# Kernel tuning notes

Hardware: AMD Instinct MI355X
Metric: run time of the kernel (lower is better)

Reference implementation:

```python
import jax, jax.numpy as jnp
import numpy as np

B, N, DIM = 1, 100_000, 512
HEADS, DIM_HEAD, M = 8, 64, 64


def setup_inputs() -> dict:
    key = jax.random.key(0)
    ks = jax.random.split(key, 9)
    s = 0.04  # ~ kaiming-ish scale for dim=512
    return {
        "x": jax.random.normal(ks[0], (B, N, DIM), dtype=jnp.float32),
        "temperature": jnp.full((1, HEADS, 1, 1), 0.5, dtype=jnp.float32),
        "w_slice": jax.random.normal(ks[1], (HEADS * M, DIM), dtype=jnp.float32) * s,
        "b_slice": jnp.zeros((HEADS * M,), dtype=jnp.float32),
        "w1": jax.random.normal(ks[2], (DIM_HEAD, DIM), dtype=jnp.float32) * s,
        "b1": jnp.zeros((DIM_HEAD,), dtype=jnp.float32),
        "wq": jax.random.normal(ks[3], (DIM_HEAD, DIM_HEAD), dtype=jnp.float32) * 0.125,
        "wk": jax.random.normal(ks[4], (DIM_HEAD, DIM_HEAD), dtype=jnp.float32) * 0.125,
        "wv": jax.random.normal(ks[5], (DIM_HEAD, DIM_HEAD), dtype=jnp.float32) * 0.125,
        "w3": jax.random.normal(ks[6], (DIM_HEAD, DIM_HEAD), dtype=jnp.float32) * 0.125,
        "b3": jnp.zeros((DIM_HEAD,), dtype=jnp.float32),
    }


def reference(x, temperature, w_slice, b_slice, w1, b1, wq, wk, wv, w3, b3):
    b, n, c = x.shape
    # slice logits: (B,N,H*M) -> (B,H,N,M)
    logits = jnp.einsum("bnc,ec->bne", x, w_slice) + b_slice
    logits = logits.reshape(b, n, HEADS, M).transpose(0, 2, 1, 3)
    temp = jnp.clip(temperature, 0.1, 5.0)
    w = jax.nn.softmax(logits / temp, axis=-1)          # (B,H,N,M)
    d = w.sum(axis=2)                                    # (B,H,M)
    # N -> M aggregation (w^T @ x per head)
    s_raw = jnp.einsum("bhnm,bnc->bhmc", w, x)          # (B,H,M,C)
    s = jnp.einsum("bhmc,dc->bhmd", s_raw / (d[..., None] + 1e-5), w1) + b1  # (B,H,M,dh)
    q = jnp.einsum("bhmd,ed->bhme", s, wq)
    k = jnp.einsum("bhmd,ed->bhme", s, wk)
    v = jnp.einsum("bhmd,ed->bhme", s, wv)
    scale = 1.0 / jnp.sqrt(jnp.asarray(DIM_HEAD, dtype=s.dtype))
    attn = jax.nn.softmax(jnp.einsum("bhme,bhle->bhml", q, k) * scale, axis=-1)
    s_att = jnp.einsum("bhml,bhle->bhme", attn, v)      # (B,H,M,dh)
    s_out = jnp.einsum("bhme,de->bhmd", s_att, w3) + b3
    # deslice: w @ s_out -> (B,H,N,dh) -> (B,N,H*dh)
    x_out = jnp.einsum("bhnm,bhmd->bhnd", w, s_out)
    return x_out.transpose(0, 2, 1, 3).reshape(b, n, HEADS * DIM_HEAD)
```

## Files before the change

kernel.cpp:

```cpp
#include <hip/hip_runtime.h>

typedef _Float16 f16;
typedef _Float16 f16x8 __attribute__((ext_vector_type(8)));
typedef _Float16 f16x4 __attribute__((ext_vector_type(4)));
typedef float    f32x4 __attribute__((ext_vector_type(4)));

#define N_TOK   100000
#define NPAD    100032
#define NT1     1563
#define NT4     1563
#define CDIM    512
#define KSTEPS  (NPAD/32)
#define K2SPL   128

#define O_WT     ((size_t)0)
#define SZ_WT    ((size_t)512*NPAD*2)
#define O_YT     (O_WT + SZ_WT)
#define SZ_YT    ((size_t)64*NPAD*2)
#define O_WFR    (O_YT + SZ_YT)
#define SZ_WFR   ((size_t)16*4*9*64*8*2)
#define O_SPP    (O_WFR + SZ_WFR)
#define SZ_SPP   ((size_t)K2SPL*32768*4)
#define O_DPP    (O_SPP + SZ_SPP)
#define SZ_DPP   ((size_t)K2SPL*512*4)
#define O_SPRE   (O_DPP + SZ_DPP)
#define SZ_SPRE  ((size_t)32768*4)
#define O_DSTD   (O_SPRE + SZ_SPRE)
#define SZ_DSTD  ((size_t)512*4)
#define O_SOUT   (O_DSTD + SZ_DSTD)

__global__ void k0_pack(const float* __restrict__ wsf, const float* __restrict__ w1f,
                        f16* __restrict__ wfr) {
    int c = blockIdx.x * 256 + threadIdx.x;
    int lane = c & 63, g = c >> 6;
    int u  = g % 9,  r = g / 9;
    int we = r & 3,  kg = r >> 2;
    int col = lane & 15, quad = lane >> 4;
    int k = kg * 32 + quad * 8;
    const float* src;
    if (u < 8) src = wsf + (size_t)(we*128 + u*16 + col) * CDIM + k;
    else       src = w1f + (size_t)(we*16  + col) * CDIM + k;
    float4 a = *(const float4*)(src);
    float4 b = *(const float4*)(src + 4);
    f16x8 h;
    h[0]=(f16)a.x; h[1]=(f16)a.y; h[2]=(f16)a.z; h[3]=(f16)a.w;
    h[4]=(f16)b.x; h[5]=(f16)b.y; h[6]=(f16)b.z; h[7]=(f16)b.w;
    *(f16x8*)(wfr + (size_t)c * 8) = h;
}

#define XROW 40
__launch_bounds__(256, 2)
__global__ void k1_slice(const float* __restrict__ x, const float* __restrict__ temperature,
                         const f16* __restrict__ wfr, const float* __restrict__ bsl,
                         f16* __restrict__ wT, f16* __restrict__ yT) {
    __shared__ f16 lX[2][64 * XROW];

    const int tid  = threadIdx.x;
    const int wave = tid >> 6;
    const int lane = tid & 63;
    const int quad = lane >> 4;
    const int col  = lane & 15;
    const int n0   = blockIdx.x * 64;

    const int srow = tid >> 2, sch = tid & 3;
    int snr = n0 + srow; if (snr > N_TOK - 1) snr = N_TOK - 1;
    const float* sbase = x + (size_t)snr * CDIM + sch * 8;

    {
        float4 a = *(const float4*)(sbase);
        float4 b = *(const float4*)(sbase + 4);
        f16x8 h;
        h[0]=(f16)a.x; h[1]=(f16)a.y; h[2]=(f16)a.z; h[3]=(f16)a.w;
        h[4]=(f16)b.x; h[5]=(f16)b.y; h[6]=(f16)b.z; h[7]=(f16)b.w;
        *(f16x8*)(&lX[0][srow * XROW + sch * 8]) = h;
    }

    f32x4 acc[4][9];
    #pragma unroll
    for (int nf = 0; nf < 4; ++nf)
        #pragma unroll
        for (int u = 0; u < 9; ++u) acc[nf][u] = f32x4{0.f,0.f,0.f,0.f};

    __syncthreads();

    #pragma unroll 2
    for (int kg = 0; kg < 16; ++kg) {
        const f16* wb = wfr + ((size_t)(kg*4 + wave) * 9) * 512 + (size_t)lane * 8;
        f16x8 bf[9];
        #pragma unroll
        for (int u = 0; u < 9; ++u) bf[u] = *(const f16x8*)(wb + u * 512);

        float4 xa, xb;
        if (kg < 15) {
            xa = *(const float4*)(sbase + (kg + 1) * 32);
            xb = *(const float4*)(sbase + (kg + 1) * 32 + 4);
        }

        const f16* xbuf = lX[kg & 1];
        f16x8 af[4];
        #pragma unroll
        for (int nf = 0; nf < 4; ++nf)
            af[nf] = *(const f16x8*)(xbuf + (nf*16 + col) * XROW + quad * 8);

        #pragma unroll
        for (int nf = 0; nf < 4; ++nf)
            #pragma unroll
            for (int u = 0; u < 9; ++u)
                acc[nf][u] = __builtin_amdgcn_mfma_f32_16x16x32_f16(af[nf], bf[u], acc[nf][u], 0, 0, 0);

        if (kg < 15) {
            f16x8 h;
            h[0]=(f16)xa.x; h[1]=(f16)xa.y; h[2]=(f16)xa.z; h[3]=(f16)xa.w;
            h[4]=(f16)xb.x; h[5]=(f16)xb.y; h[6]=(f16)xb.z; h[7]=(f16)xb.w;
            *(f16x8*)(&lX[(kg + 1) & 1][srow * XROW + sch * 8]) = h;
        }
        __syncthreads();
    }

    #pragma unroll
    for (int u = 0; u < 8; ++u) {
        float b = bsl[wave*128 + u*16 + col];
        #pragma unroll
        for (int nf = 0; nf < 4; ++nf)
            #pragma unroll
            for (int r = 0; r < 4; ++r) acc[nf][u][r] += b;
    }
    float invt[2];
    #pragma unroll
    for (int hh = 0; hh < 2; ++hh) {
        float tv = temperature[wave*2 + hh];
        tv = fminf(fmaxf(tv, 0.1f), 5.0f);
        invt[hh] = 1.0f / tv;
    }

    #pragma unroll
    for (int nf = 0; nf < 4; ++nf) {
        const int nb = n0 + nf*16 + quad*4;
        #pragma unroll
        for (int hh = 0; hh < 2; ++hh) {
            float mx[4];
            #pragma unroll
            for (int r = 0; r < 4; ++r) {
                float m01 = fmaxf(acc[nf][hh*4+0][r], acc[nf][hh*4+1][r]);
                float m23 = fmaxf(acc[nf][hh*4+2][r], acc[nf][hh*4+3][r]);
                mx[r] = fmaxf(m01, m23);
            }
            #pragma unroll
            for (int d = 1; d < 16; d <<= 1)
                #pragma unroll
                for (int r = 0; r < 4; ++r) mx[r] = fmaxf(mx[r], __shfl_xor(mx[r], d));
            float sm[4] = {0.f, 0.f, 0.f, 0.f};
            #pragma unroll
            for (int uu = 0; uu < 4; ++uu)
                #pragma unroll
                for (int r = 0; r < 4; ++r) {
                    float ev = __expf((acc[nf][hh*4+uu][r] - mx[r]) * invt[hh]);
                    acc[nf][hh*4+uu][r] = ev;
                    sm[r] += ev;
                }
            #pragma unroll
            for (int d = 1; d < 16; d <<= 1)
                #pragma unroll
                for (int r = 0; r < 4; ++r) sm[r] += __shfl_xor(sm[r], d);
            #pragma unroll
            for (int r = 0; r < 4; ++r) sm[r] = 1.0f / sm[r];
            #pragma unroll
            for (int uu = 0; uu < 4; ++uu) {
                f16x4 pk;
                #pragma unroll
                for (int r = 0; r < 4; ++r) {
                    int n = nb + r;
                    float wv = (n < N_TOK) ? acc[nf][hh*4+uu][r] * sm[r] : 0.0f;
                    pk[r] = (f16)wv;
                }
                int e = wave*128 + (hh*4 + uu)*16 + col;
                *(f16x4*)(wT + (size_t)e * NPAD + nb) = pk;
            }
        }
        {
            f16x4 pk;
            #pragma unroll
            for (int r = 0; r < 4; ++r) {
                int n = nb + r;
                pk[r] = (n < N_TOK) ? (f16)acc[nf][8][r] : (f16)0.f;
            }
            *(f16x4*)(yT + (size_t)(wave*16 + col) * NPAD + nb) = pk;
        }
    }
}

__launch_bounds__(256, 3)
__global__ void k2_spre(const f16* __restrict__ wT, const f16* __restrict__ yT,
                        float* __restrict__ spp, float* __restrict__ dpp) {
    const int tid = threadIdx.x, wave = tid >> 6, lane = tid & 63;
    const int quad = lane >> 4, col = lane & 15;
    const int slot = blockIdx.x >> 1, ehalf = blockIdx.x & 1;
    const int ebase = ehalf * 256 + wave * 64;

    f32x4 acc[4][4];
    float dac[4];
    #pragma unroll
    for (int u = 0; u < 4; ++u) {
        dac[u] = 0.f;
        #pragma unroll
        for (int v = 0; v < 4; ++v) acc[u][v] = f32x4{0.f,0.f,0.f,0.f};
    }
    for (int ks = slot; ks < KSTEPS; ks += K2SPL) {
        int nb = ks*32 + quad*8;
        f16x8 bf[4];
        #pragma unroll
        for (int v = 0; v < 4; ++v)
            bf[v] = *(const f16x8*)(yT + (size_t)(v*16 + col)*NPAD + nb);
        #pragma unroll
        for (int u = 0; u < 4; ++u) {
            f16x8 af = *(const f16x8*)(wT + (size_t)(ebase + u*16 + col)*NPAD + nb);
            #pragma unroll
            for (int v = 0; v < 4; ++v)
                acc[u][v] = __builtin_amdgcn_mfma_f32_16x16x32_f16(af, bf[v], acc[u][v], 0, 0, 0);
            float s = 0.f;
            #pragma unroll
            for (int j = 0; j < 8; ++j) s += (float)af[j];
            dac[u] += s;
        }
    }
    #pragma unroll
    for (int u = 0; u < 4; ++u) {
        dac[u] += __shfl_xor(dac[u], 16);
        dac[u] += __shfl_xor(dac[u], 32);
    }
    if (quad == 0) {
        #pragma unroll
        for (int u = 0; u < 4; ++u)
            dpp[slot*512 + ebase + u*16 + col] = dac[u];
    }
    float* dst = spp + (size_t)slot * 32768 + (size_t)ehalf * 16384;
    #pragma unroll
    for (int u = 0; u < 4; ++u)
        #pragma unroll
        for (int v = 0; v < 4; ++v)
            *(f32x4*)(dst + (size_t)((wave*4 + u)*4 + v)*256 + (size_t)lane*4) = acc[u][v];
}

__global__ void k2r_reduce(const float* __restrict__ spp, const float* __restrict__ dpp,
                           float* __restrict__ spre, float* __restrict__ dstd) {
    int i = blockIdx.x*256 + threadIdx.x;
    float s = 0.f;
    for (int p = 0; p < K2SPL; ++p) s += spp[(size_t)p*32768 + i];
    int r = i & 3, L = (i >> 2) & 63, v = (i >> 8) & 3, t = (i >> 10) & 15, eh = i >> 14;
    int e = eh*256 + (t >> 2)*64 + (t & 3)*16 + (L >> 4)*4 + r;
    int d = v*16 + (L & 15);
    spre[e*64 + d] = s;
    if (i < 512) {
        float tt = 0.f;
        for (int p = 0; p < K2SPL; ++p) tt += dpp[p*512 + i];
        dstd[i] = tt;
    }
}

__global__ void k3_attn(const float* __restrict__ spre, const float* __restrict__ dstd,
                        const float* __restrict__ b1, const float* __restrict__ wq,
                        const float* __restrict__ wk, const float* __restrict__ wv,
                        const float* __restrict__ w3, const float* __restrict__ b3,
                        f16* __restrict__ sout) {
    __shared__ float wa[64][65], wb[64][65], wc[64][65];
    __shared__ float ss[64][65], qq[64][65], kk[64][65], vv[64][65], sc[64][65];
    const int h = blockIdx.x, tid = threadIdx.x;

    for (int i = tid; i < 4096; i += 256) {
        int r = i >> 6, c = i & 63;
        wa[r][c] = wq[i];
        wb[r][c] = wk[i];
        wc[r][c] = wv[i];
        ss[r][c] = spre[h*4096 + i] / (dstd[h*64 + r] + 1e-5f) + b1[c];
    }
    __syncthreads();

    #pragma unroll
    for (int it = 0; it < 16; ++it) {
        int m = it*4 + (tid >> 6), e = tid & 63;
        float aq = 0.f, ak = 0.f, av = 0.f;
        #pragma unroll 8
        for (int d = 0; d < 64; ++d) {
            float sv = ss[m][d];
            aq += sv * wa[e][d];
            ak += sv * wb[e][d];
            av += sv * wc[e][d];
        }
        qq[m][e] = aq; kk[m][e] = ak; vv[m][e] = av;
    }
    __syncthreads();

    for (int i = tid; i < 4096; i += 256) wa[i >> 6][i & 63] = w3[i];
    #pragma unroll
    for (int it = 0; it < 16; ++it) {
        int m = it*4 + (tid >> 6), l = tid & 63;
        float a = 0.f;
        #pragma unroll 8
        for (int e = 0; e < 64; ++e) a += qq[m][e] * kk[l][e];
        sc[m][l] = a * 0.125f;
    }
    __syncthreads();

    if (tid < 64) {
        int m = tid;
        float mx = -1e30f;
        #pragma unroll 8
        for (int l = 0; l < 64; ++l) mx = fmaxf(mx, sc[m][l]);
        float sm = 0.f;
        #pragma unroll 8
        for (int l = 0; l < 64; ++l) { float ev = __expf(sc[m][l] - mx); sc[m][l] = ev; sm += ev; }
        float rs = 1.0f / sm;
        #pragma unroll 8
        for (int l = 0; l < 64; ++l) sc[m][l] *= rs;
    }
    __syncthreads();

    #pragma unroll
    for (int it = 0; it < 16; ++it) {
        int m = it*4 + (tid >> 6), e = tid & 63;
        float a = 0.f;
        #pragma unroll 8
        for (int l = 0; l < 64; ++l) a += sc[m][l] * vv[l][e];
        ss[m][e] = a;
    }
    __syncthreads();

    #pragma unroll
    for (int it = 0; it < 16; ++it) {
        int d = it*4 + (tid >> 6), m = tid & 63;
        float a = b3[d];
        #pragma unroll 8
        for (int e = 0; e < 64; ++e) a += ss[m][e] * wa[d][e];
        sout[(h*64 + d)*64 + m] = (f16)a;
    }
}

__launch_bounds__(256, 2)
__global__ void k4_deslice(const f16* __restrict__ wT, const f16* __restrict__ sout,
                           float* __restrict__ out) {
    __shared__ f16 ldsW[512*68];
    const int tid = threadIdx.x, wave = tid >> 6, lane = tid & 63;
    const int quad = lane >> 4, col = lane & 15;
    const int n0 = blockIdx.x * 64;

    #pragma unroll
    for (int i = 0; i < 32; ++i) {
        int id = tid + i*256;
        int e = id >> 4, p = id & 15;
        f16x4 v = *(const f16x4*)(wT + (size_t)e*NPAD + n0 + p*4);
        *(f16x4*)(ldsW + (size_t)e*68 + p*4) = v;
    }
    __syncthreads();

    f32x4 acc[2][4][4];
    #pragma unroll
    for (int hh = 0; hh < 2; ++hh)
        #pragma unroll
        for (int t = 0; t < 4; ++t)
            #pragma unroll
            for (int v = 0; v < 4; ++v) acc[hh][t][v] = f32x4{0.f,0.f,0.f,0.f};

    #pragma unroll
    for (int hh = 0; hh < 2; ++hh) {
        int h = wave*2 + hh;
        #pragma unroll
        for (int ks = 0; ks < 2; ++ks) {
            f16x8 af[4];
            #pragma unroll
            for (int t = 0; t < 4; ++t) {
                f16x8 a;
                #pragma unroll
                for (int j = 0; j < 8; ++j)
                    a[j] = ldsW[(size_t)(h*64 + ks*32 + quad*8 + j)*68 + t*16 + col];
                af[t] = a;
            }
            #pragma unroll
            for (int v = 0; v < 4; ++v) {
                f16x8 bf = *(const f16x8*)(sout + (size_t)(h*64 + v*16 + col)*64 + ks*32 + quad*8);
                #pragma unroll
                for (int t = 0; t < 4; ++t)
                    acc[hh][t][v] = __builtin_amdgcn_mfma_f32_16x16x32_f16(af[t], bf, acc[hh][t][v], 0, 0, 0);
            }
        }
    }

    #pragma unroll
    for (int hh = 0; hh < 2; ++hh) {
        int h = wave*2 + hh;
        #pragma unroll
        for (int t = 0; t < 4; ++t)
            #pragma unroll
            for (int v = 0; v < 4; ++v)
                #pragma unroll
                for (int r = 0; r < 4; ++r) {
                    int n = n0 + t*16 + quad*4 + r;
                    if (n < N_TOK)
                        out[(size_t)n*512 + h*64 + v*16 + col] = acc[hh][t][v][r];
                }
    }
}

extern "C" void kernel_launch(void* const* d_in, const int* in_sizes, int n_in,
                              void* d_out, int out_size, void* d_ws, size_t ws_size,
                              hipStream_t stream) {
    const float* x           = (const float*)d_in[0];
    const float* temperature = (const float*)d_in[1];
    const float* w_slice     = (const float*)d_in[2];
    const float* b_slice     = (const float*)d_in[3];
    const float* w1          = (const float*)d_in[4];
    const float* b1          = (const float*)d_in[5];
    const float* wq          = (const float*)d_in[6];
    const float* wk          = (const float*)d_in[7];
    const float* wv          = (const float*)d_in[8];
    const float* w3          = (const float*)d_in[9];
    const float* b3          = (const float*)d_in[10];
    float* out = (float*)d_out;
    char*  ws  = (char*)d_ws;

    f16*   wT    = (f16*)(ws + O_WT);
    f16*   yT    = (f16*)(ws + O_YT);
    f16*   wfr   = (f16*)(ws + O_WFR);
    float* spp   = (float*)(ws + O_SPP);
    float* dpp   = (float*)(ws + O_DPP);
    float* spre  = (float*)(ws + O_SPRE);
    float* dstd  = (float*)(ws + O_DSTD);
    f16*   sout  = (f16*)(ws + O_SOUT);

    k0_pack<<<144, 256, 0, stream>>>(w_slice, w1, wfr);
    k1_slice<<<NT1, 256, 0, stream>>>(x, temperature, wfr, b_slice, wT, yT);
    k2_spre<<<K2SPL*2, 256, 0, stream>>>(wT, yT, spp, dpp);
    k2r_reduce<<<128, 256, 0, stream>>>(spp, dpp, spre, dstd);
    k3_attn<<<8, 256, 0, stream>>>(spre, dstd, b1, wq, wk, wv, w3, b3, sout);
    k4_deslice<<<NT4, 256, 0, stream>>>(wT, sout, out);
}
```

Before: 620.6 us.

## Stage slice weights through LDS and add N-major copy for deslice

k1 now stages the transposed softmax weights in LDS and writes them to global as coalesced 16-byte rows. When the workspace is large enough, it also writes an N-major copy (wN) so a new k4_wn kernel can read contiguous MFMA A-fragments without an LDS transpose. k2 splits the E dimension four ways to raise occupancy, and k3 runs with 1024 threads. The cost is an extra 100MB fp16 write in k1 and larger LDS use there, and the new path runs only if ws_size allows it.

```diff
diff --git a/kernel.cpp b/kernel.cpp
--- a/kernel.cpp
+++ b/kernel.cpp
@@ -8,7 +8,6 @@
 #define N_TOK   100000
 #define NPAD    100032
 #define NT1     1563
-#define NT4     1563
 #define CDIM    512
 #define KSTEPS  (NPAD/32)
 #define K2SPL   128
@@ -28,6 +27,9 @@
 #define O_DSTD   (O_SPRE + SZ_SPRE)
 #define SZ_DSTD  ((size_t)512*4)
 #define O_SOUT   (O_DSTD + SZ_DSTD)
+#define SZ_SOUT  ((size_t)8*64*64*2)
+#define O_WN     (O_SOUT + SZ_SOUT)
+#define SZ_WN    ((size_t)NPAD*512*2)
 
 __global__ void k0_pack(const float* __restrict__ wsf, const float* __restrict__ w1f,
                         f16* __restrict__ wfr) {
@@ -49,11 +51,16 @@
 }
 
 #define XROW 40
+#define TPITCH 72
+#define NPITCH 536
 __launch_bounds__(256, 2)
 __global__ void k1_slice(const float* __restrict__ x, const float* __restrict__ temperature,
                          const f16* __restrict__ wfr, const float* __restrict__ bsl,
-                         f16* __restrict__ wT, f16* __restrict__ yT) {
-    __shared__ f16 lX[2][64 * XROW];
+                         f16* __restrict__ wT, f16* __restrict__ yT, f16* __restrict__ wN) {
+    __shared__ f16 smem[512 * TPITCH];
+    f16* lX = smem;
+    f16* lT = smem;
+    f16* lN = smem;
 
     const int tid  = threadIdx.x;
     const int wave = tid >> 6;
@@ -72,7 +79,7 @@
         f16x8 h;
         h[0]=(f16)a.x; h[1]=(f16)a.y; h[2]=(f16)a.z; h[3]=(f16)a.w;
         h[4]=(f16)b.x; h[5]=(f16)b.y; h[6]=(f16)b.z; h[7]=(f16)b.w;
-        *(f16x8*)(&lX[0][srow * XROW + sch * 8]) = h;
+        *(f16x8*)(&lX[srow * XROW + sch * 8]) = h;
     }
 
     f32x4 acc[4][9];
@@ -96,7 +103,7 @@
             xb = *(const float4*)(sbase + (kg + 1) * 32 + 4);
         }
 
-        const f16* xbuf = lX[kg & 1];
+        const f16* xbuf = lX + (kg & 1) * (64 * XROW);
         f16x8 af[4];
         #pragma unroll
         for (int nf = 0; nf < 4; ++nf)
@@ -112,7 +119,7 @@
             f16x8 h;
             h[0]=(f16)xa.x; h[1]=(f16)xa.y; h[2]=(f16)xa.z; h[3]=(f16)xa.w;
             h[4]=(f16)xb.x; h[5]=(f16)xb.y; h[6]=(f16)xb.z; h[7]=(f16)xb.w;
-            *(f16x8*)(&lX[(kg + 1) & 1][srow * XROW + sch * 8]) = h;
+            *(f16x8*)(&lX[((kg + 1) & 1) * (64 * XROW) + srow * XROW + sch * 8]) = h;
         }
         __syncthreads();
     }
@@ -135,7 +142,7 @@
 
     #pragma unroll
     for (int nf = 0; nf < 4; ++nf) {
-        const int nb = n0 + nf*16 + quad*4;
+        const int nloc = nf*16 + quad*4;
         #pragma unroll
         for (int hh = 0; hh < 2; ++hh) {
             float mx[4];
@@ -169,38 +176,72 @@
                 f16x4 pk;
                 #pragma unroll
                 for (int r = 0; r < 4; ++r) {
-                    int n = nb + r;
-                    float wv = (n < N_TOK) ? acc[nf][hh*4+uu][r] * sm[r] : 0.0f;
-                    pk[r] = (f16)wv;
+                    acc[nf][hh*4+uu][r] *= sm[r];
+                    int n = n0 + nloc + r;
+                    pk[r] = (n < N_TOK) ? (f16)acc[nf][hh*4+uu][r] : (f16)0.f;
                 }
                 int e = wave*128 + (hh*4 + uu)*16 + col;
-                *(f16x4*)(wT + (size_t)e * NPAD + nb) = pk;
+                *(f16x4*)(lT + (size_t)e*TPITCH + nloc) = pk;
             }
         }
         {
             f16x4 pk;
             #pragma unroll
             for (int r = 0; r < 4; ++r) {
-                int n = nb + r;
+                int n = n0 + nloc + r;
                 pk[r] = (n < N_TOK) ? (f16)acc[nf][8][r] : (f16)0.f;
             }
-            *(f16x4*)(yT + (size_t)(wave*16 + col) * NPAD + nb) = pk;
-        }
-    }
-}
-
-__launch_bounds__(256, 3)
+            *(f16x4*)(yT + (size_t)(wave*16 + col) * NPAD + n0 + nloc) = pk;
+        }
+    }
+    __syncthreads();
+
+    #pragma unroll
+    for (int i = 0; i < 16; ++i) {
+        int id = tid + i*256;
+        int e = id >> 3, p = id & 7;
+        f16x8 v = *(const f16x8*)(lT + (size_t)e*TPITCH + p*8);
+        *(f16x8*)(wT + (size_t)e*NPAD + n0 + p*8) = v;
+    }
+
+    if (wN != nullptr) {
+        __syncthreads();
+        #pragma unroll
+        for (int nf = 0; nf < 4; ++nf) {
+            const int nloc = nf*16 + quad*4;
+            #pragma unroll
+            for (int hh = 0; hh < 2; ++hh)
+                #pragma unroll
+                for (int uu = 0; uu < 4; ++uu) {
+                    int e = wave*128 + (hh*4 + uu)*16 + col;
+                    #pragma unroll
+                    for (int r = 0; r < 4; ++r)
+                        lN[(size_t)(nloc + r)*NPITCH + e] = (f16)acc[nf][hh*4+uu][r];
+                }
+        }
+        __syncthreads();
+        #pragma unroll
+        for (int i = 0; i < 16; ++i) {
+            int id = tid + i*256;
+            int n = id >> 6, ec = id & 63;
+            f16x8 v = *(const f16x8*)(lN + (size_t)n*NPITCH + ec*8);
+            *(f16x8*)(wN + (size_t)(n0 + n)*512 + ec*8) = v;
+        }
+    }
+}
+
+__launch_bounds__(256, 4)
 __global__ void k2_spre(const f16* __restrict__ wT, const f16* __restrict__ yT,
                         float* __restrict__ spp, float* __restrict__ dpp) {
     const int tid = threadIdx.x, wave = tid >> 6, lane = tid & 63;
     const int quad = lane >> 4, col = lane & 15;
-    const int slot = blockIdx.x >> 1, ehalf = blockIdx.x & 1;
-    const int ebase = ehalf * 256 + wave * 64;
-
-    f32x4 acc[4][4];
-    float dac[4];
-    #pragma unroll
-    for (int u = 0; u < 4; ++u) {
+    const int slot = blockIdx.x >> 2, equad = blockIdx.x & 3;
+    const int ebase = equad * 128 + wave * 32;
+
+    f32x4 acc[2][4];
+    float dac[2];
+    #pragma unroll
+    for (int u = 0; u < 2; ++u) {
         dac[u] = 0.f;
         #pragma unroll
         for (int v = 0; v < 4; ++v) acc[u][v] = f32x4{0.f,0.f,0.f,0.f};
@@ -212,7 +253,7 @@
         for (int v = 0; v < 4; ++v)
             bf[v] = *(const f16x8*)(yT + (size_t)(v*16 + col)*NPAD + nb);
         #pragma unroll
-        for (int u = 0; u < 4; ++u) {
+        for (int u = 0; u < 2; ++u) {
             f16x8 af = *(const f16x8*)(wT + (size_t)(ebase + u*16 + col)*NPAD + nb);
             #pragma unroll
             for (int v = 0; v < 4; ++v)
@@ -224,21 +265,21 @@
         }
     }
     #pragma unroll
-    for (int u = 0; u < 4; ++u) {
+    for (int u = 0; u < 2; ++u) {
         dac[u] += __shfl_xor(dac[u], 16);
         dac[u] += __shfl_xor(dac[u], 32);
     }
     if (quad == 0) {
         #pragma unroll
-        for (int u = 0; u < 4; ++u)
+        for (int u = 0; u < 2; ++u)
             dpp[slot*512 + ebase + u*16 + col] = dac[u];
     }
-    float* dst = spp + (size_t)slot * 32768 + (size_t)ehalf * 16384;
-    #pragma unroll
-    for (int u = 0; u < 4; ++u)
+    float* dst = spp + (size_t)slot * 32768 + (size_t)equad * 8192;
+    #pragma unroll
+    for (int u = 0; u < 2; ++u)
         #pragma unroll
         for (int v = 0; v < 4; ++v)
-            *(f32x4*)(dst + (size_t)((wave*4 + u)*4 + v)*256 + (size_t)lane*4) = acc[u][v];
+            *(f32x4*)(dst + (size_t)((wave*2 + u)*4 + v)*256 + (size_t)lane*4) = acc[u][v];
 }
 
 __global__ void k2r_reduce(const float* __restrict__ spp, const float* __restrict__ dpp,
@@ -246,8 +287,8 @@
     int i = blockIdx.x*256 + threadIdx.x;
     float s = 0.f;
     for (int p = 0; p < K2SPL; ++p) s += spp[(size_t)p*32768 + i];
-    int r = i & 3, L = (i >> 2) & 63, v = (i >> 8) & 3, t = (i >> 10) & 15, eh = i >> 14;
-    int e = eh*256 + (t >> 2)*64 + (t & 3)*16 + (L >> 4)*4 + r;
+    int r = i & 3, L = (i >> 2) & 63, v = (i >> 8) & 3, g = (i >> 10) & 7, eq = (i >> 13) & 3;
+    int e = eq*128 + (g >> 1)*32 + (g & 1)*16 + (L >> 4)*4 + r;
     int d = v*16 + (L & 15);
     spre[e*64 + d] = s;
     if (i < 512) {
@@ -266,7 +307,7 @@
     __shared__ float ss[64][65], qq[64][65], kk[64][65], vv[64][65], sc[64][65];
     const int h = blockIdx.x, tid = threadIdx.x;
 
-    for (int i = tid; i < 4096; i += 256) {
+    for (int i = tid; i < 4096; i += 1024) {
         int r = i >> 6, c = i & 63;
         wa[r][c] = wq[i];
         wb[r][c] = wk[i];
@@ -276,8 +317,8 @@
     __syncthreads();
 
     #pragma unroll
-    for (int it = 0; it < 16; ++it) {
-        int m = it*4 + (tid >> 6), e = tid & 63;
+    for (int it = 0; it < 4; ++it) {
+        int m = it*16 + (tid >> 6), e = tid & 63;
         float aq = 0.f, ak = 0.f, av = 0.f;
         #pragma unroll 8
         for (int d = 0; d < 64; ++d) {
@@ -290,10 +331,10 @@
     }
     __syncthreads();
 
-    for (int i = tid; i < 4096; i += 256) wa[i >> 6][i & 63] = w3[i];
-    #pragma unroll
-    for (int it = 0; it < 16; ++it) {
-        int m = it*4 + (tid >> 6), l = tid & 63;
+    for (int i = tid; i < 4096; i += 1024) wa[i >> 6][i & 63] = w3[i];
+    #pragma unroll
+    for (int it = 0; it < 4; ++it) {
+        int m = it*16 + (tid >> 6), l = tid & 63;
         float a = 0.f;
         #pragma unroll 8
         for (int e = 0; e < 64; ++e) a += qq[m][e] * kk[l][e];
@@ -316,8 +357,8 @@
     __syncthreads();
 
     #pragma unroll
-    for (int it = 0; it < 16; ++it) {
-        int m = it*4 + (tid >> 6), e = tid & 63;
+    for (int it = 0; it < 4; ++it) {
+        int m = it*16 + (tid >> 6), e = tid & 63;
         float a = 0.f;
         #pragma unroll 8
         for (int l = 0; l < 64; ++l) a += sc[m][l] * vv[l][e];
@@ -326,12 +367,63 @@
     __syncthreads();
 
     #pragma unroll
-    for (int it = 0; it < 16; ++it) {
-        int d = it*4 + (tid >> 6), m = tid & 63;
+    for (int it = 0; it < 4; ++it) {
+        int d = it*16 + (tid >> 6), m = tid & 63;
         float a = b3[d];
         #pragma unroll 8
         for (int e = 0; e < 64; ++e) a += ss[m][e] * wa[d][e];
         sout[(h*64 + d)*64 + m] = (f16)a;
+    }
+}
+
+__launch_bounds__(256, 3)
+__global__ void k4_wn(const f16* __restrict__ wN, const f16* __restrict__ sout,
+                      float* __restrict__ out) {
+    const int tid = threadIdx.x, wave = tid >> 6, lane = tid & 63;
+    const int quad = lane >> 4, col = lane & 15;
+    const int n0 = blockIdx.x * 32;
+
+    f32x4 acc[2][2][4];
+    #pragma unroll
+    for (int hh = 0; hh < 2; ++hh)
+        #pragma unroll
+        for (int t = 0; t < 2; ++t)
+            #pragma unroll
+            for (int v = 0; v < 4; ++v) acc[hh][t][v] = f32x4{0.f,0.f,0.f,0.f};
+
+    #pragma unroll
+    for (int hh = 0; hh < 2; ++hh) {
+        int h = wave*2 + hh;
+        #pragma unroll
+        for (int ks = 0; ks < 2; ++ks) {
+            f16x8 af[2], bf[4];
+            #pragma unroll
+            for (int t = 0; t < 2; ++t)
+                af[t] = *(const f16x8*)(wN + (size_t)(n0 + t*16 + col)*512 + h*64 + ks*32 + quad*8);
+            #pragma unroll
+            for (int v = 0; v < 4; ++v)
+                bf[v] = *(const f16x8*)(sout + (size_t)(h*64 + v*16 + col)*64 + ks*32 + quad*8);
+            #pragma unroll
+            for (int t = 0; t < 2; ++t)
+                #pragma unroll
+                for (int v = 0; v < 4; ++v)
+                    acc[hh][t][v] = __builtin_amdgcn_mfma_f32_16x16x32_f16(af[t], bf[v], acc[hh][t][v], 0, 0, 0);
+        }
+    }
+
+    #pragma unroll
+    for (int hh = 0; hh < 2; ++hh) {
+        int h = wave*2 + hh;
+        #pragma unroll
+        for (int t = 0; t < 2; ++t)
+            #pragma unroll
+            for (int v = 0; v < 4; ++v)
+                #pragma unroll
+                for (int r = 0; r < 4; ++r) {
+                    int n = n0 + t*16 + quad*4 + r;
+                    if (n < N_TOK)
+                        out[(size_t)n*512 + h*64 + v*16 + col] = acc[hh][t][v][r];
+                }
     }
 }
 
@@ -426,10 +518,14 @@
     float* dstd  = (float*)(ws + O_DSTD);
     f16*   sout  = (f16*)(ws + O_SOUT);
 
+    const int use_wn = (ws_size >= (O_WN + SZ_WN)) ? 1 : 0;
+    f16* wN = use_wn ? (f16*)(ws + O_WN) : nullptr;
+
     k0_pack<<<144, 256, 0, stream>>>(w_slice, w1, wfr);
-    k1_slice<<<NT1, 256, 0, stream>>>(x, temperature, wfr, b_slice, wT, yT);
-    k2_spre<<<K2SPL*2, 256, 0, stream>>>(wT, yT, spp, dpp);
+    k1_slice<<<NT1, 256, 0, stream>>>(x, temperature, wfr, b_slice, wT, yT, wN);
+    k2_spre<<<K2SPL*4, 256, 0, stream>>>(wT, yT, spp, dpp);
     k2r_reduce<<<128, 256, 0, stream>>>(spp, dpp, spre, dstd);
-    k3_attn<<<8, 256, 0, stream>>>(spre, dstd, b1, wq, wk, wv, w3, b3, sout);
-    k4_deslice<<<NT4, 256, 0, stream>>>(wT, sout, out);
-}
+    k3_attn<<<8, 1024, 0, stream>>>(spre, dstd, b1, wq, wk, wv, w3, b3, sout);
+    if (use_wn) k4_wn<<<KSTEPS, 256, 0, stream>>>(wN, sout, out);
+    else        k4_deslice<<<NT1, 256, 0, stream>>>(wT, sout, out);
+}
```

Result: slower. 634.8 us (+2.3%).
